# Kernel optimization log

Hardware: AMD Instinct MI355X
Metric: run time of the kernel (lower is better)

The kernel has to match this reference:

```python
import jax, jax.numpy as jnp
import numpy as np

N_NODES = 100000
N_EDGES = 1600000
F_IN = 64
HID = 64
N_CLASSES = 45
N_GRAPHS = 256


def gcn_conv(x, src, dst, W, b, n):
    # GCNConv with added self-loops and symmetric normalization (PyG semantics)
    h = x @ W  # [N, H]
    deg = jax.ops.segment_sum(jnp.ones(src.shape[0], h.dtype), dst, num_segments=n) + 1.0
    dinv = jax.lax.rsqrt(deg)  # deg^{-1/2}, deg >= 1 due to self loops
    coef = dinv[src] * dinv[dst]  # [E]
    msg = h[src] * coef[:, None]  # gather + scale
    agg = jax.ops.segment_sum(msg, dst, num_segments=n)  # scatter-add to dst
    agg = agg + h * (dinv * dinv)[:, None]  # self-loop contribution
    return agg + b


def setup_inputs() -> dict:
    key = jax.random.key(0)
    ks = jax.random.split(key, 12)
    x = jax.random.normal(ks[0], (N_NODES, F_IN), dtype=jnp.float32)
    edge_index = jax.random.randint(ks[1], (2, N_EDGES), 0, N_NODES, dtype=jnp.int32)
    batch = jnp.sort(jax.random.randint(ks[2], (N_NODES,), 0, N_GRAPHS, dtype=jnp.int32))
    s1 = 1.0 / np.sqrt(F_IN)
    s2 = 1.0 / np.sqrt(HID)
    W1 = jax.random.uniform(ks[3], (F_IN, HID), jnp.float32, -s1, s1)
    b1 = jnp.zeros((HID,), jnp.float32)
    W2 = jax.random.uniform(ks[4], (HID, HID), jnp.float32, -s2, s2)
    b2 = jnp.zeros((HID,), jnp.float32)
    W3 = jax.random.uniform(ks[5], (HID, HID), jnp.float32, -s2, s2)
    b3 = jnp.zeros((HID,), jnp.float32)
    Wl = jax.random.uniform(ks[6], (HID, N_CLASSES), jnp.float32, -s2, s2)
    bl = jnp.zeros((N_CLASSES,), jnp.float32)
    return {"x": x, "edge_index": edge_index, "batch": batch,
            "W1": W1, "b1": b1, "W2": W2, "b2": b2, "W3": W3, "b3": b3,
            "Wl": Wl, "bl": bl}


def reference(x, edge_index, batch, W1, b1, W2, b2, W3, b3, Wl, bl):
    n = x.shape[0]
    src, dst = edge_index[0], edge_index[1]
    h = jax.nn.relu(gcn_conv(x, src, dst, W1, b1, n))
    h = jax.nn.relu(gcn_conv(h, src, dst, W2, b2, n))
    h = gcn_conv(h, src, dst, W3, b3, n)
    # global mean pool over graph segments
    sums = jax.ops.segment_sum(h, batch, num_segments=N_GRAPHS)  # [G, H]
    cnts = jax.ops.segment_sum(jnp.ones(n, h.dtype), batch, num_segments=N_GRAPHS)
    pooled = sums / jnp.maximum(cnts, 1.0)[:, None]
    # dropout is identity in eval mode
    return pooled @ Wl + bl  # [G, num_classes]
```

## Files before the change

### kernel.cpp

```cpp
#include <hip/hip_runtime.h>
#include <hip/hip_bf16.h>

#define N_NODES   100000
#define N_EDGES   1600000
#define F_IN      64
#define HID       64
#define N_CLASSES 45
#define N_GRAPHS  256
#define SB        392
#define NPB       256
#define CAP       4608
#define WPB       72
#define CHUNK     4096
#define NCHUNK    391
#define NZB       256
#define GEMM_GRID 3125
#define ZLEN4     3204096

__device__ __forceinline__ float rl_f(float v, int k) {
    return __uint_as_float(__builtin_amdgcn_readlane(__float_as_uint(v), k));
}
__device__ __forceinline__ int rl_i(int v, int k) {
    return __builtin_amdgcn_readlane(v, k);
}
__device__ __forceinline__ unsigned short f2bf(float x) {
    unsigned u = __float_as_uint(x);
    unsigned r = u + 0x7FFFu + ((u >> 16) & 1u);
    return (unsigned short)(r >> 16);
}
__device__ __forceinline__ float bf2f(unsigned short h) {
    return __uint_as_float(((unsigned)h) << 16);
}

__global__ __launch_bounds__(256) void k_front(const int* __restrict__ src, const int* __restrict__ dst,
                                               int* __restrict__ bcur, int* __restrict__ binned,
                                               const float* __restrict__ x, const float* __restrict__ W1,
                                               unsigned short* __restrict__ P, float* __restrict__ zbase) {
    int bid = blockIdx.x;
    int t   = threadIdx.x;
    if (bid < NCHUNK) {
        __shared__ int stg[CHUNK];
        __shared__ unsigned short bkt[CHUNK];
        __shared__ int h[512], cur[512], off[512];
        __shared__ int ps[256];
        h[t] = 0; h[t + 256] = 0;
        __syncthreads();
        int base4 = bid * (CHUNK / 4);
        #pragma unroll
        for (int i = 0; i < CHUNK / 1024; i++) {
            int e4 = base4 + i * 256 + t;
            if (e4 < N_EDGES / 4) {
                int4 d = ((const int4*)dst)[e4];
                atomicAdd(&h[d.x >> 8], 1);
                atomicAdd(&h[d.y >> 8], 1);
                atomicAdd(&h[d.z >> 8], 1);
                atomicAdd(&h[d.w >> 8], 1);
            }
        }
        __syncthreads();
        int a0 = h[2 * t], a1 = h[2 * t + 1];
        ps[t] = a0 + a1;
        __syncthreads();
        for (int o = 1; o < 256; o <<= 1) {
            int v = (t >= o) ? ps[t - o] : 0;
            __syncthreads();
            if (t >= o) ps[t] += v;
            __syncthreads();
        }
        int pex = ps[t] - (a0 + a1);
        int e0 = pex, e1 = pex + a0;
        cur[2 * t] = e0; cur[2 * t + 1] = e1;
        if (2 * t < SB && a0 > 0)
            off[2 * t] = (2 * t) * CAP + atomicAdd(&bcur[2 * t], a0) - e0;
        if (2 * t + 1 < SB && a1 > 0)
            off[2 * t + 1] = (2 * t + 1) * CAP + atomicAdd(&bcur[2 * t + 1], a1) - e1;
        __syncthreads();
        int total = ps[255];
        #pragma unroll
        for (int i = 0; i < CHUNK / 1024; i++) {
            int e4 = base4 + i * 256 + t;
            if (e4 < N_EDGES / 4) {
                int4 d  = ((const int4*)dst)[e4];
                int4 s4 = ((const int4*)src)[e4];
                int q;
                q = atomicAdd(&cur[d.x >> 8], 1); stg[q] = s4.x | ((d.x & 255) << 17); bkt[q] = (unsigned short)(d.x >> 8);
                q = atomicAdd(&cur[d.y >> 8], 1); stg[q] = s4.y | ((d.y & 255) << 17); bkt[q] = (unsigned short)(d.y >> 8);
                q = atomicAdd(&cur[d.z >> 8], 1); stg[q] = s4.z | ((d.z & 255) << 17); bkt[q] = (unsigned short)(d.z >> 8);
                q = atomicAdd(&cur[d.w >> 8], 1); stg[q] = s4.w | ((d.w & 255) << 17); bkt[q] = (unsigned short)(d.w >> 8);
            }
        }
        __syncthreads();
        for (int i = t; i < total; i += 256) {
            int b = bkt[i];
            binned[off[b] + i] = stg[i];
        }
    } else if (bid < NCHUNK + NZB) {
        float4 z = make_float4(0.f, 0.f, 0.f, 0.f);
        float4* zp = (float4*)zbase;
        int zb = bid - NCHUNK;
        for (long i = (long)zb * 256 + t; i < (long)ZLEN4; i += (long)NZB * 256)
            zp[i] = z;
    } else {
        int gbid = bid - NCHUNK - NZB;
        int lane = t & 63;
        int wv   = t >> 6;
        int base = gbid * 32 + wv * 8;
        float xr[8], acc[8];
        #pragma unroll
        for (int r = 0; r < 8; r++) {
            xr[r]  = x[(size_t)(base + r) * 64 + lane];
            acc[r] = 0.f;
        }
        for (int kb = 0; kb < 64; kb += 8) {
            float wb[8];
            #pragma unroll
            for (int j = 0; j < 8; j++) wb[j] = W1[(kb + j) * 64 + lane];
            #pragma unroll
            for (int j = 0; j < 8; j++) {
                #pragma unroll
                for (int r = 0; r < 8; r++)
                    acc[r] = fmaf(rl_f(xr[r], kb + j), wb[j], acc[r]);
            }
        }
        #pragma unroll
        for (int r = 0; r < 8; r++)
            P[(size_t)(base + r) * 64 + lane] = f2bf(acc[r]);
    }
}

__global__ __launch_bounds__(256) void k_bcsr(const int* __restrict__ binned, const int* __restrict__ bcur,
                                              float* __restrict__ dinv, float* __restrict__ dinv2,
                                              int* __restrict__ csr) {
    __shared__ int h[NPB];
    __shared__ int ts[NPB];
    int t = threadIdx.x;
    int b = blockIdx.x;
    int nb0  = b << 8;
    int ebeg = b * CAP;
    int ecnt = bcur[b]; if (ecnt > CAP) ecnt = CAP;
    h[t] = 0;
    __syncthreads();
    for (int i = t; i < ecnt; i += 256)
        atomicAdd(&h[binned[ebeg + i] >> 17], 1);
    __syncthreads();
    int c = h[t];
    ts[t] = c;
    __syncthreads();
    for (int o = 1; o < 256; o <<= 1) {
        int v = (t >= o) ? ts[t - o] : 0;
        __syncthreads();
        if (t >= o) ts[t] += v;
        __syncthreads();
    }
    int excl = ts[t] - c + ebeg;
    int n = nb0 + t;
    if (n < N_NODES) {
        float inv = 1.0f / (float)(c + 1);
        dinv2[n] = inv;
        dinv[n]  = sqrtf(inv);
    }
    __syncthreads();
    h[t] = excl;
    __syncthreads();
    for (int i = t; i < ecnt; i += 256) {
        int p = binned[ebeg + i];
        int q = atomicAdd(&h[p >> 17], 1);
        csr[q] = p;
    }
}

template<bool POOLI>
__global__ __launch_bounds__(256) void k_gemm(const float* __restrict__ E,
                                              unsigned short* P,
                                              const float* __restrict__ W,
                                              const float* __restrict__ bprev,
                                              const float* __restrict__ bcurr,
                                              const float* __restrict__ dinv2,
                                              const int* __restrict__ batch,
                                              float* __restrict__ pool) {
    int lane = threadIdx.x & 63;
    int wv   = threadIdx.x >> 6;
    int base = blockIdx.x * 32 + wv * 8;
    float bp = bprev[lane];
    float xr[8], acc[8];
    #pragma unroll
    for (int r = 0; r < 8; r++) {
        int n = base + r;
        float hp = bf2f(P[(size_t)n * 64 + lane]);
        float a  = E[(size_t)n * 64 + lane] + fmaf(hp, dinv2[n], bp);
        xr[r]  = fmaxf(a, 0.f);
        acc[r] = 0.f;
    }
    for (int kb = 0; kb < 64; kb += 8) {
        float wb[8];
        #pragma unroll
        for (int j = 0; j < 8; j++) wb[j] = W[(kb + j) * 64 + lane];
        #pragma unroll
        for (int j = 0; j < 8; j++) {
            #pragma unroll
            for (int r = 0; r < 8; r++)
                acc[r] = fmaf(rl_f(xr[r], kb + j), wb[j], acc[r]);
        }
    }
    #pragma unroll
    for (int r = 0; r < 8; r++)
        P[(size_t)(base + r) * 64 + lane] = f2bf(acc[r]);
    if (POOLI) {
        float bv = bcurr[lane];
        float d2[8];
        #pragma unroll
        for (int r = 0; r < 8; r++) d2[r] = dinv2[base + r];
        int g0 = batch[base], g7 = batch[base + 7];
        if (g0 == g7) {
            float s = 0.f;
            #pragma unroll
            for (int r = 0; r < 8; r++) s += fmaf(acc[r], d2[r], bv);
            atomicAdd(&pool[g0 * 64 + lane], s);
        } else {
            #pragma unroll
            for (int r = 0; r < 8; r++) {
                int g = batch[base + r];
                atomicAdd(&pool[g * 64 + lane], fmaf(acc[r], d2[r], bv));
            }
        }
    }
}

template<bool POOLEP>
__global__ __launch_bounds__(256, 8) void k_agge(const unsigned short* __restrict__ Hbuf,
                                                 const int* __restrict__ csr,
                                                 const int* __restrict__ bcur,
                                                 const float* __restrict__ dinv,
                                                 const int* __restrict__ batch,
                                                 float* __restrict__ Out) {
    int wv   = threadIdx.x >> 6;
    int lane = threadIdx.x & 63;
    int wid  = blockIdx.x * 4 + wv;
    int b    = wid / WPB;
    int lw   = wid - b * WPB;
    int used = bcur[b]; if (used > CAP) used = CAP;
    int e0   = lw * 64;
    int rem  = used - e0;
    if (rem <= 0) return;
    if (rem > 64) rem = 64;
    int base = b * CAP + e0;

    int p = 0;
    float cv = 0.f;
    if (lane < rem) {
        p  = csr[base + lane];
        cv = dinv[p & 0x1FFFF];
    }
    int sv = p & 0x1FFFF;
    int dv = p >> 17;

    auto flush = [&](int dl, float a) {
        int dst = (b << 8) + dl;
        if (dst < N_NODES) {
            float val = dinv[dst] * a;
            if (POOLEP) {
                int g = batch[dst];
                atomicAdd(&Out[g * 64 + lane], val);
            } else {
                atomicAdd(&Out[(size_t)dst * 64 + lane], val);
            }
        }
    };

    int dprev = rl_i(dv, 0);
    float acc = 0.f;
    int j = 0;
    for (; j + 8 <= rem; j += 8) {
        int   s0 = rl_i(sv, j),     s1 = rl_i(sv, j + 1);
        int   s2 = rl_i(sv, j + 2), s3 = rl_i(sv, j + 3);
        int   s4 = rl_i(sv, j + 4), s5 = rl_i(sv, j + 5);
        int   s6 = rl_i(sv, j + 6), s7 = rl_i(sv, j + 7);
        float c0 = rl_f(cv, j),     c1 = rl_f(cv, j + 1);
        float c2 = rl_f(cv, j + 2), c3 = rl_f(cv, j + 3);
        float c4 = rl_f(cv, j + 4), c5 = rl_f(cv, j + 5);
        float c6 = rl_f(cv, j + 6), c7 = rl_f(cv, j + 7);
        int   d0 = rl_i(dv, j),     d1 = rl_i(dv, j + 1);
        int   d2 = rl_i(dv, j + 2), d3 = rl_i(dv, j + 3);
        int   d4 = rl_i(dv, j + 4), d5 = rl_i(dv, j + 5);
        int   d6 = rl_i(dv, j + 6), d7 = rl_i(dv, j + 7);
        unsigned short u0 = Hbuf[(size_t)s0 * 64 + lane];
        unsigned short u1 = Hbuf[(size_t)s1 * 64 + lane];
        unsigned short u2 = Hbuf[(size_t)s2 * 64 + lane];
        unsigned short u3 = Hbuf[(size_t)s3 * 64 + lane];
        unsigned short u4 = Hbuf[(size_t)s4 * 64 + lane];
        unsigned short u5 = Hbuf[(size_t)s5 * 64 + lane];
        unsigned short u6 = Hbuf[(size_t)s6 * 64 + lane];
        unsigned short u7 = Hbuf[(size_t)s7 * 64 + lane];
        if (d0 != dprev) { flush(dprev, acc); acc = 0.f; dprev = d0; }
        acc = fmaf(bf2f(u0), c0, acc);
        if (d1 != dprev) { flush(dprev, acc); acc = 0.f; dprev = d1; }
        acc = fmaf(bf2f(u1), c1, acc);
        if (d2 != dprev) { flush(dprev, acc); acc = 0.f; dprev = d2; }
        acc = fmaf(bf2f(u2), c2, acc);
        if (d3 != dprev) { flush(dprev, acc); acc = 0.f; dprev = d3; }
        acc = fmaf(bf2f(u3), c3, acc);
        if (d4 != dprev) { flush(dprev, acc); acc = 0.f; dprev = d4; }
        acc = fmaf(bf2f(u4), c4, acc);
        if (d5 != dprev) { flush(dprev, acc); acc = 0.f; dprev = d5; }
        acc = fmaf(bf2f(u5), c5, acc);
        if (d6 != dprev) { flush(dprev, acc); acc = 0.f; dprev = d6; }
        acc = fmaf(bf2f(u6), c6, acc);
        if (d7 != dprev) { flush(dprev, acc); acc = 0.f; dprev = d7; }
        acc = fmaf(bf2f(u7), c7, acc);
    }
    for (; j < rem; j++) {
        int   s0 = rl_i(sv, j);
        float c0 = rl_f(cv, j);
        int   d0 = rl_i(dv, j);
        unsigned short u0 = Hbuf[(size_t)s0 * 64 + lane];
        if (d0 != dprev) { flush(dprev, acc); acc = 0.f; dprev = d0; }
        acc = fmaf(bf2f(u0), c0, acc);
    }
    flush(dprev, acc);
}

__device__ __forceinline__ int lbound(const int* __restrict__ a, int n, int v) {
    int lo = 0, hi = n;
    while (lo < hi) { int m = (lo + hi) >> 1; if (a[m] < v) lo = m + 1; else hi = m; }
    return lo;
}

__global__ __launch_bounds__(64) void k_cls(const float* __restrict__ pool, const int* __restrict__ batch,
                                            const float* __restrict__ Wl, const float* __restrict__ bl,
                                            float* __restrict__ out) {
    __shared__ float pm[64];
    __shared__ int bounds[2];
    int g = blockIdx.x;
    int t = threadIdx.x;
    if (t < 2) bounds[t] = lbound(batch, N_NODES, g + t);
    __syncthreads();
    float cnt = (float)(bounds[1] - bounds[0]);
    pm[t] = pool[g * 64 + t] / fmaxf(cnt, 1.0f);
    __syncthreads();
    if (t < N_CLASSES) {
        float o = bl[t];
        #pragma unroll
        for (int k = 0; k < HID; k++) o = fmaf(pm[k], Wl[k * N_CLASSES + t], o);
        out[g * N_CLASSES + t] = o;
    }
}


extern "C" void kernel_launch(void* const* d_in, const int* in_sizes, int n_in,
                              void* d_out, int out_size, void* d_ws, size_t ws_size,
                              hipStream_t stream) {
    const float* x     = (const float*)d_in[0];
    const int*   eidx  = (const int*)  d_in[1];
    const int*   batch = (const int*)  d_in[2];
    const float* W1 = (const float*)d_in[3];
    const float* b1 = (const float*)d_in[4];
    const float* W2 = (const float*)d_in[5];
    const float* b2 = (const float*)d_in[6];
    const float* W3 = (const float*)d_in[7];
    const float* b3 = (const float*)d_in[8];
    const float* Wl = (const float*)d_in[9];
    const float* bl = (const float*)d_in[10];
    const int* src = eidx;
    const int* dst = eidx + N_EDGES;

    char* p = (char*)d_ws;
    auto alloc = [&](size_t bytes) -> void* {
        void* r = (void*)p;
        p += (bytes + 255) & ~(size_t)255;
        return r;
    };
    float* dinv  = (float*)alloc((size_t)N_NODES * 4);
    float* dinv2 = (float*)alloc((size_t)N_NODES * 4);
    int*   csr   = (int*)  alloc((size_t)SB * CAP * 4);
    unsigned short* P = (unsigned short*)alloc((size_t)N_NODES * 64 * 2);
    float* E1    = (float*)alloc((size_t)N_NODES * 64 * 4);
    float* pool  = (float*)alloc((size_t)N_GRAPHS * 64 * 4);
    float* E2    = (float*)alloc((size_t)N_NODES * 64 * 4);
    int*   bcur  = (int*)  alloc((size_t)SB * 4);
    int*   binned = (int*) alloc((size_t)SB * CAP * 4);

    const int agge_grid  = SB * WPB / 4;
    const int front_grid = NCHUNK + NZB + GEMM_GRID;

    hipMemsetAsync(bcur, 0, (size_t)SB * 4, stream);
    k_front<<<front_grid, 256, 0, stream>>>(src, dst, bcur, binned, x, W1, P, E1);
    k_bcsr <<<SB, 256, 0, stream>>>(binned, bcur, dinv, dinv2, csr);

    k_agge<false><<<agge_grid, 256, 0, stream>>>(P, csr, bcur, dinv, batch, E1);
    k_gemm<false><<<GEMM_GRID, 256, 0, stream>>>(E1, P, W2, b1, nullptr, dinv2, batch, nullptr);
    k_agge<false><<<agge_grid, 256, 0, stream>>>(P, csr, bcur, dinv, batch, E2);
    k_gemm<true ><<<GEMM_GRID, 256, 0, stream>>>(E2, P, W3, b2, b3, dinv2, batch, pool);
    k_agge<true ><<<agge_grid, 256, 0, stream>>>(P, csr, bcur, dinv, batch, pool);

    k_cls<<<N_GRAPHS, 64, 0, stream>>>(pool, batch, Wl, bl, (float*)d_out);
}
```

Before: 378.4 us.

## Move E2/pool zeroing into first aggregation launch and batch 16 gathers before accumulate

The zero-fill work that the front kernel did for both E1 and the E2+pool region is split. The front kernel now clears only E1, and extra blocks appended to the first aggregation launch clear E2 and pool. This shortens the front kernel's critical path. The aggregation inner loop is also restructured to issue 16 independent bf16 gathers before the dependent accumulate/flush chain, which raises memory-level parallelism at the cost of more registers.

```diff
diff --git a/kernel.cpp b/kernel.cpp
--- a/kernel.cpp
+++ b/kernel.cpp
@@ -13,9 +13,12 @@
 #define WPB       72
 #define CHUNK     4096
 #define NCHUNK    391
-#define NZB       256
+#define NZB       192
 #define GEMM_GRID 3125
-#define ZLEN4     3204096
+#define AGGE_GRID 7056
+#define NZB2      192
+#define ZLEN4_F   1600000
+#define ZLEN4_A   1604096
 
 __device__ __forceinline__ float rl_f(float v, int k) {
     return __uint_as_float(__builtin_amdgcn_readlane(__float_as_uint(v), k));
@@ -98,7 +101,7 @@
         float4 z = make_float4(0.f, 0.f, 0.f, 0.f);
         float4* zp = (float4*)zbase;
         int zb = bid - NCHUNK;
-        for (long i = (long)zb * 256 + t; i < (long)ZLEN4; i += (long)NZB * 256)
+        for (long i = (long)zb * 256 + t; i < (long)ZLEN4_F; i += (long)NZB * 256)
             zp[i] = z;
     } else {
         int gbid = bid - NCHUNK - NZB;
@@ -226,15 +229,25 @@
     }
 }
 
-template<bool POOLEP>
+template<bool POOLEP, bool ZROLE>
 __global__ __launch_bounds__(256, 8) void k_agge(const unsigned short* __restrict__ Hbuf,
                                                  const int* __restrict__ csr,
                                                  const int* __restrict__ bcur,
                                                  const float* __restrict__ dinv,
                                                  const int* __restrict__ batch,
-                                                 float* __restrict__ Out) {
-    int wv   = threadIdx.x >> 6;
-    int lane = threadIdx.x & 63;
+                                                 float* __restrict__ Out,
+                                                 float* __restrict__ zbase) {
+    int t = threadIdx.x;
+    if (ZROLE && blockIdx.x >= AGGE_GRID) {
+        float4 z = make_float4(0.f, 0.f, 0.f, 0.f);
+        float4* zp = (float4*)zbase;
+        int zb = blockIdx.x - AGGE_GRID;
+        for (long i = (long)zb * 256 + t; i < (long)ZLEN4_A; i += (long)NZB2 * 256)
+            zp[i] = z;
+        return;
+    }
+    int wv   = t >> 6;
+    int lane = t & 63;
     int wid  = blockIdx.x * 4 + wv;
     int b    = wid / WPB;
     int lw   = wid - b * WPB;
@@ -270,43 +283,20 @@
     int dprev = rl_i(dv, 0);
     float acc = 0.f;
     int j = 0;
-    for (; j + 8 <= rem; j += 8) {
-        int   s0 = rl_i(sv, j),     s1 = rl_i(sv, j + 1);
-        int   s2 = rl_i(sv, j + 2), s3 = rl_i(sv, j + 3);
-        int   s4 = rl_i(sv, j + 4), s5 = rl_i(sv, j + 5);
-        int   s6 = rl_i(sv, j + 6), s7 = rl_i(sv, j + 7);
-        float c0 = rl_f(cv, j),     c1 = rl_f(cv, j + 1);
-        float c2 = rl_f(cv, j + 2), c3 = rl_f(cv, j + 3);
-        float c4 = rl_f(cv, j + 4), c5 = rl_f(cv, j + 5);
-        float c6 = rl_f(cv, j + 6), c7 = rl_f(cv, j + 7);
-        int   d0 = rl_i(dv, j),     d1 = rl_i(dv, j + 1);
-        int   d2 = rl_i(dv, j + 2), d3 = rl_i(dv, j + 3);
-        int   d4 = rl_i(dv, j + 4), d5 = rl_i(dv, j + 5);
-        int   d6 = rl_i(dv, j + 6), d7 = rl_i(dv, j + 7);
-        unsigned short u0 = Hbuf[(size_t)s0 * 64 + lane];
-        unsigned short u1 = Hbuf[(size_t)s1 * 64 + lane];
-        unsigned short u2 = Hbuf[(size_t)s2 * 64 + lane];
-        unsigned short u3 = Hbuf[(size_t)s3 * 64 + lane];
-        unsigned short u4 = Hbuf[(size_t)s4 * 64 + lane];
-        unsigned short u5 = Hbuf[(size_t)s5 * 64 + lane];
-        unsigned short u6 = Hbuf[(size_t)s6 * 64 + lane];
-        unsigned short u7 = Hbuf[(size_t)s7 * 64 + lane];
-        if (d0 != dprev) { flush(dprev, acc); acc = 0.f; dprev = d0; }
-        acc = fmaf(bf2f(u0), c0, acc);
-        if (d1 != dprev) { flush(dprev, acc); acc = 0.f; dprev = d1; }
-        acc = fmaf(bf2f(u1), c1, acc);
-        if (d2 != dprev) { flush(dprev, acc); acc = 0.f; dprev = d2; }
-        acc = fmaf(bf2f(u2), c2, acc);
-        if (d3 != dprev) { flush(dprev, acc); acc = 0.f; dprev = d3; }
-        acc = fmaf(bf2f(u3), c3, acc);
-        if (d4 != dprev) { flush(dprev, acc); acc = 0.f; dprev = d4; }
-        acc = fmaf(bf2f(u4), c4, acc);
-        if (d5 != dprev) { flush(dprev, acc); acc = 0.f; dprev = d5; }
-        acc = fmaf(bf2f(u5), c5, acc);
-        if (d6 != dprev) { flush(dprev, acc); acc = 0.f; dprev = d6; }
-        acc = fmaf(bf2f(u6), c6, acc);
-        if (d7 != dprev) { flush(dprev, acc); acc = 0.f; dprev = d7; }
-        acc = fmaf(bf2f(u7), c7, acc);
+    for (; j + 16 <= rem; j += 16) {
+        unsigned short u[16];
+        #pragma unroll
+        for (int i = 0; i < 16; i++) {
+            int s = rl_i(sv, j + i);
+            u[i] = Hbuf[(size_t)s * 64 + lane];
+        }
+        #pragma unroll
+        for (int i = 0; i < 16; i++) {
+            int   d = rl_i(dv, j + i);
+            float c = rl_f(cv, j + i);
+            if (d != dprev) { flush(dprev, acc); acc = 0.f; dprev = d; }
+            acc = fmaf(bf2f(u[i]), c, acc);
+        }
     }
     for (; j < rem; j++) {
         int   s0 = rl_i(sv, j);
@@ -379,18 +369,17 @@
     int*   bcur  = (int*)  alloc((size_t)SB * 4);
     int*   binned = (int*) alloc((size_t)SB * CAP * 4);
 
-    const int agge_grid  = SB * WPB / 4;
     const int front_grid = NCHUNK + NZB + GEMM_GRID;
 
     hipMemsetAsync(bcur, 0, (size_t)SB * 4, stream);
     k_front<<<front_grid, 256, 0, stream>>>(src, dst, bcur, binned, x, W1, P, E1);
     k_bcsr <<<SB, 256, 0, stream>>>(binned, bcur, dinv, dinv2, csr);
 
-    k_agge<false><<<agge_grid, 256, 0, stream>>>(P, csr, bcur, dinv, batch, E1);
+    k_agge<false, true ><<<AGGE_GRID + NZB2, 256, 0, stream>>>(P, csr, bcur, dinv, batch, E1, pool);
     k_gemm<false><<<GEMM_GRID, 256, 0, stream>>>(E1, P, W2, b1, nullptr, dinv2, batch, nullptr);
-    k_agge<false><<<agge_grid, 256, 0, stream>>>(P, csr, bcur, dinv, batch, E2);
+    k_agge<false, false><<<AGGE_GRID, 256, 0, stream>>>(P, csr, bcur, dinv, batch, E2, nullptr);
     k_gemm<true ><<<GEMM_GRID, 256, 0, stream>>>(E2, P, W3, b2, b3, dinv2, batch, pool);
-    k_agge<true ><<<agge_grid, 256, 0, stream>>>(P, csr, bcur, dinv, batch, pool);
+    k_agge<true , false><<<AGGE_GRID, 256, 0, stream>>>(P, csr, bcur, dinv, batch, pool, nullptr);
 
     k_cls<<<N_GRAPHS, 64, 0, stream>>>(pool, batch, Wl, bl, (float*)d_out);
 }
```

After: 369.8 us. -2.3%, faster.

## Precompute edge coefficients into CSR and split zeroing across kernels

Applied to the files above, without the earlier changes.

CSR construction is split into a degree/offset kernel and a fill kernel that stores each edge with its precomputed source dinv coefficient as an int2. The three aggregation passes then read the coefficient directly instead of doing a random gather of dinv per edge. The zeroing of E2 and pool moves from the front kernel into extra blocks of the first aggregation launch, which shortens the front kernel. In exchange there is one more kernel launch and the CSR array doubles in size, so every aggregation pass reads more bytes.

```diff
diff --git a/kernel.cpp b/kernel.cpp
--- a/kernel.cpp
+++ b/kernel.cpp
@@ -13,9 +13,12 @@
 #define WPB       72
 #define CHUNK     4096
 #define NCHUNK    391
-#define NZB       256
+#define NZB       192
 #define GEMM_GRID 3125
-#define ZLEN4     3204096
+#define AGGE_GRID 7056
+#define NZB2      192
+#define ZLEN4_F   1600000
+#define ZLEN4_A   1604096
 
 __device__ __forceinline__ float rl_f(float v, int k) {
     return __uint_as_float(__builtin_amdgcn_readlane(__float_as_uint(v), k));
@@ -98,7 +101,7 @@
         float4 z = make_float4(0.f, 0.f, 0.f, 0.f);
         float4* zp = (float4*)zbase;
         int zb = bid - NCHUNK;
-        for (long i = (long)zb * 256 + t; i < (long)ZLEN4; i += (long)NZB * 256)
+        for (long i = (long)zb * 256 + t; i < (long)ZLEN4_F; i += (long)NZB * 256)
             zp[i] = z;
     } else {
         int gbid = bid - NCHUNK - NZB;
@@ -128,9 +131,9 @@
     }
 }
 
-__global__ __launch_bounds__(256) void k_bcsr(const int* __restrict__ binned, const int* __restrict__ bcur,
+__global__ __launch_bounds__(256) void k_bdeg(const int* __restrict__ binned, const int* __restrict__ bcur,
                                               float* __restrict__ dinv, float* __restrict__ dinv2,
-                                              int* __restrict__ csr) {
+                                              int* __restrict__ nodeoff) {
     __shared__ int h[NPB];
     __shared__ int ts[NPB];
     int t = threadIdx.x;
@@ -158,14 +161,27 @@
         float inv = 1.0f / (float)(c + 1);
         dinv2[n] = inv;
         dinv[n]  = sqrtf(inv);
-    }
-    __syncthreads();
-    h[t] = excl;
+        nodeoff[n] = excl;
+    }
+}
+
+__global__ __launch_bounds__(256) void k_bfill(const int* __restrict__ binned, const int* __restrict__ bcur,
+                                               const int* __restrict__ nodeoff, const float* __restrict__ dinv,
+                                               int2* __restrict__ csr) {
+    __shared__ int cur[NPB];
+    int t = threadIdx.x;
+    int b = blockIdx.x;
+    int nb0  = b << 8;
+    int ebeg = b * CAP;
+    int ecnt = bcur[b]; if (ecnt > CAP) ecnt = CAP;
+    int n = nb0 + t;
+    cur[t] = (n < N_NODES) ? nodeoff[n] : 0;
     __syncthreads();
     for (int i = t; i < ecnt; i += 256) {
-        int p = binned[ebeg + i];
-        int q = atomicAdd(&h[p >> 17], 1);
-        csr[q] = p;
+        int p  = binned[ebeg + i];
+        float cs = dinv[p & 0x1FFFF];
+        int q = atomicAdd(&cur[p >> 17], 1);
+        csr[q] = make_int2(p, __float_as_int(cs));
     }
 }
 
@@ -226,15 +242,25 @@
     }
 }
 
-template<bool POOLEP>
+template<bool POOLEP, bool ZROLE>
 __global__ __launch_bounds__(256, 8) void k_agge(const unsigned short* __restrict__ Hbuf,
-                                                 const int* __restrict__ csr,
+                                                 const int2* __restrict__ csr,
                                                  const int* __restrict__ bcur,
                                                  const float* __restrict__ dinv,
                                                  const int* __restrict__ batch,
-                                                 float* __restrict__ Out) {
-    int wv   = threadIdx.x >> 6;
-    int lane = threadIdx.x & 63;
+                                                 float* __restrict__ Out,
+                                                 float* __restrict__ zbase) {
+    int t = threadIdx.x;
+    if (ZROLE && blockIdx.x >= AGGE_GRID) {
+        float4 z = make_float4(0.f, 0.f, 0.f, 0.f);
+        float4* zp = (float4*)zbase;
+        int zb = blockIdx.x - AGGE_GRID;
+        for (long i = (long)zb * 256 + t; i < (long)ZLEN4_A; i += (long)NZB2 * 256)
+            zp[i] = z;
+        return;
+    }
+    int wv   = t >> 6;
+    int lane = t & 63;
     int wid  = blockIdx.x * 4 + wv;
     int b    = wid / WPB;
     int lw   = wid - b * WPB;
@@ -248,8 +274,9 @@
     int p = 0;
     float cv = 0.f;
     if (lane < rem) {
-        p  = csr[base + lane];
-        cv = dinv[p & 0x1FFFF];
+        int2 pc = csr[base + lane];
+        p  = pc.x;
+        cv = __int_as_float(pc.y);
     }
     int sv = p & 0x1FFFF;
     int dv = p >> 17;
@@ -371,7 +398,8 @@
     };
     float* dinv  = (float*)alloc((size_t)N_NODES * 4);
     float* dinv2 = (float*)alloc((size_t)N_NODES * 4);
-    int*   csr   = (int*)  alloc((size_t)SB * CAP * 4);
+    int*   nodeoff = (int*)alloc((size_t)N_NODES * 4);
+    int2*  csr   = (int2*) alloc((size_t)SB * CAP * 8);
     unsigned short* P = (unsigned short*)alloc((size_t)N_NODES * 64 * 2);
     float* E1    = (float*)alloc((size_t)N_NODES * 64 * 4);
     float* pool  = (float*)alloc((size_t)N_GRAPHS * 64 * 4);
@@ -379,18 +407,18 @@
     int*   bcur  = (int*)  alloc((size_t)SB * 4);
     int*   binned = (int*) alloc((size_t)SB * CAP * 4);
 
-    const int agge_grid  = SB * WPB / 4;
     const int front_grid = NCHUNK + NZB + GEMM_GRID;
 
     hipMemsetAsync(bcur, 0, (size_t)SB * 4, stream);
     k_front<<<front_grid, 256, 0, stream>>>(src, dst, bcur, binned, x, W1, P, E1);
-    k_bcsr <<<SB, 256, 0, stream>>>(binned, bcur, dinv, dinv2, csr);
-
-    k_agge<false><<<agge_grid, 256, 0, stream>>>(P, csr, bcur, dinv, batch, E1);
+    k_bdeg <<<SB, 256, 0, stream>>>(binned, bcur, dinv, dinv2, nodeoff);
+    k_bfill<<<SB, 256, 0, stream>>>(binned, bcur, nodeoff, dinv, csr);
+
+    k_agge<false, true ><<<AGGE_GRID + NZB2, 256, 0, stream>>>(P, csr, bcur, dinv, batch, E1, pool);
     k_gemm<false><<<GEMM_GRID, 256, 0, stream>>>(E1, P, W2, b1, nullptr, dinv2, batch, nullptr);
-    k_agge<false><<<agge_grid, 256, 0, stream>>>(P, csr, bcur, dinv, batch, E2);
+    k_agge<false, false><<<AGGE_GRID, 256, 0, stream>>>(P, csr, bcur, dinv, batch, E2, nullptr);
     k_gemm<true ><<<GEMM_GRID, 256, 0, stream>>>(E2, P, W3, b2, b3, dinv2, batch, pool);
-    k_agge<true ><<<agge_grid, 256, 0, stream>>>(P, csr, bcur, dinv, batch, pool);
+    k_agge<true , false><<<AGGE_GRID, 256, 0, stream>>>(P, csr, bcur, dinv, batch, pool, nullptr);
 
     k_cls<<<N_GRAPHS, 64, 0, stream>>>(pool, batch, Wl, bl, (float*)d_out);
 }
```

New measurement: 377.5 us. About the same (-0.2%).
